# Kernel optimization log

Measured on AMD Instinct MI355X. Metric: run time of the kernel, lower is better.

The kernel has to match this reference:

```python
import jax, jax.numpy as jnp
import numpy as np

# hyperparameters from init_kwargs
TEMP = 0.05
MOMENTUM = 0.2
ALPHA = 0.9
TEMP_DIST = 0.6
LAMBDA1 = 1.0
LAMBDA2 = 1.0
EPS_CONS = 2.0
NUM_SAMPLES = 8192
NUM_FEATURES = 2048
B = 256
K = 20
EPS = 1e-12


def setup_inputs() -> dict:
    key = jax.random.key(0)
    ks = jax.random.split(key, 8)
    inputs0 = jax.random.normal(ks[0], (B, NUM_FEATURES), dtype=jnp.float32)
    logits0 = jax.random.normal(ks[1], (B, NUM_SAMPLES), dtype=jnp.float32)
    logits1 = jax.random.normal(ks[2], (B, NUM_SAMPLES), dtype=jnp.float32)
    targets = jax.random.randint(ks[3], (B,), 0, NUM_SAMPLES, dtype=jnp.int32)
    indexes = jnp.arange(B, dtype=jnp.int32)  # global idx == batch idx (identity idx2bidx)
    neighbors = jax.random.randint(ks[4], (B, K), 0, B, dtype=jnp.int32)
    neighbor_dists = jax.random.uniform(ks[5], (B, K), dtype=jnp.float32)
    rampup = jnp.ones((), dtype=jnp.float32)
    features = jax.random.normal(ks[6], (NUM_SAMPLES, NUM_FEATURES), dtype=jnp.float32)
    features = features / jnp.linalg.norm(features, axis=1, keepdims=True)
    return {
        'inputs0': inputs0, 'logits0': logits0, 'logits1': logits1,
        'targets': targets, 'indexes': indexes, 'neighbors': neighbors,
        'neighbor_dists': neighbor_dists, 'rampup': rampup, 'features': features,
    }


def reference(inputs0, logits0, logits1, targets, indexes, neighbors,
              neighbor_dists, rampup, features):
    # F.normalize(inputs[0], dim=1)
    x = inputs0 / jnp.maximum(jnp.linalg.norm(inputs0, axis=1, keepdims=True), EPS)

    # CM forward: scores against memory bank, scaled by temperature
    outputs = (x @ features.T) / TEMP                      # [B, S]
    logp = jax.nn.log_softmax(outputs, axis=-1)
    loss_nce = -jnp.mean(jnp.take_along_axis(logp, targets[:, None], axis=1))

    targets_onehot = jax.nn.one_hot(targets, NUM_SAMPLES, dtype=logits0.dtype)

    # neighbor gathering: indexes = arange(B) so idx2bidx is identity; every
    # neighbor in [0,B) passes the `nb in indexes` filter.
    p0 = jax.nn.softmax(logits0, axis=-1)[neighbors]       # [B, K, S]
    p1 = jax.nn.softmax(logits1, axis=-1)[neighbors]       # [B, K, S]
    # loop appends logits0-row then logits1-row per neighbor -> interleave
    p = jnp.stack([p0, p1], axis=2).reshape(B, 2 * K, NUM_SAMPLES)
    d2 = jnp.repeat(neighbor_dists, 2, axis=1)             # [B, 2K] (d,d pairs)
    w = jax.nn.softmax(d2 / TEMP_DIST, axis=1)             # [B, 2K]
    logits_neighbors1 = jnp.einsum('bk,bks->bs', w, p)     # [B, S]

    # KL branch: neighbors with dist <= eps_consistency (all, since eps=2.0)
    mask = (neighbor_dists <= EPS_CONS).astype(p0.dtype)   # [B, K]
    cnt = jnp.maximum(mask.sum(axis=1, keepdims=True), 1.0)
    logits_neighbors1_KL = jnp.einsum('bk,bks->bs', mask, p0) / cnt  # [B, S]

    refined = ALPHA * targets_onehot + (1.0 - ALPHA) * jax.lax.stop_gradient(logits_neighbors1)
    loss_ce = jnp.mean(jnp.sum(-refined * jax.nn.log_softmax(logits0, axis=-1), axis=1))

    # KLDivLoss(logsoftmax(logits1).detach(), target) with batchmean reduction
    lp1 = jax.lax.stop_gradient(jax.nn.log_softmax(logits1, axis=-1))
    t = logits_neighbors1_KL
    kl = jnp.sum(jnp.where(t > 0, t * (jnp.log(jnp.maximum(t, EPS)) - lp1), 0.0)) / B

    # CM momentum memory-bank scatter update (backward side-effect in torch);
    # equivalent to the sequential loop when targets are unique in the batch.
    upd = MOMENTUM * features[targets] + (1.0 - MOMENTUM) * x
    upd = upd / jnp.maximum(jnp.linalg.norm(upd, axis=1, keepdims=True), EPS)
    new_features = features.at[targets].set(upd)

    return (loss_nce, LAMBDA1 * loss_ce, LAMBDA2 * rampup * kl, new_features)
```

## Files before the change

### kernel.cpp

```cpp
#include <hip/hip_runtime.h>
#include <cmath>

#define NB 256
#define NS 8192
#define NF 2048
#define NK 20

typedef _Float16 half8 __attribute__((ext_vector_type(8)));
typedef _Float16 half4 __attribute__((ext_vector_type(4)));
typedef float f32x4 __attribute__((ext_vector_type(4)));

__device__ __forceinline__ void async16(const void* g, void* l) {
  __builtin_amdgcn_global_load_lds(
      (const __attribute__((address_space(1))) unsigned int*)g,
      (__attribute__((address_space(3))) unsigned int*)l, 16, 0, 0);
}

__device__ __forceinline__ float waveSum(float v) {
#pragma unroll
  for (int off = 32; off > 0; off >>= 1) v += __shfl_xor(v, off, 64);
  return v;
}
__device__ __forceinline__ float waveMax(float v) {
#pragma unroll
  for (int off = 32; off > 0; off >>= 1) v = fmaxf(v, __shfl_xor(v, off, 64));
  return v;
}

__global__ __launch_bounds__(256) void prep(
    const float* __restrict__ in0, const float* __restrict__ logits0,
    const float* __restrict__ logits1, _Float16* __restrict__ P,
    _Float16* __restrict__ xh, float* __restrict__ alpha,
    float* __restrict__ mll, float* __restrict__ loss) {
  __shared__ float redA[4], redB[4];
  int tid = threadIdx.x, blk = blockIdx.x;
  int wave = tid >> 6, lane = tid & 63;

  if (blk < 512) {
    if (blk == 0 && tid < 3) loss[tid] = 0.0f;
    int r = blk;
    const float* src = (r < NB) ? logits0 : logits1;
    const float4* row = (const float4*)(src + (size_t)(r & (NB - 1)) * NS);
    float4 v[8];
    float mx = -1e30f;
#pragma unroll
    for (int i = 0; i < 8; ++i) {
      v[i] = row[tid + i * 256];
      mx = fmaxf(mx, fmaxf(fmaxf(v[i].x, v[i].y), fmaxf(v[i].z, v[i].w)));
    }
    float wv = waveMax(mx);
    if (lane == 0) redA[wave] = wv;
    __syncthreads();
    float m = fmaxf(fmaxf(redA[0], redA[1]), fmaxf(redA[2], redA[3]));
    float em = expf(m);
    float se = 0.0f;
    half4* prow = (half4*)(P + (size_t)r * NS);
#pragma unroll
    for (int i = 0; i < 8; ++i) {
      float e0 = expf(v[i].x - m), e1 = expf(v[i].y - m);
      float e2 = expf(v[i].z - m), e3 = expf(v[i].w - m);
      se += (e0 + e1) + (e2 + e3);
      half4 h;
      h[0] = (_Float16)(e0 * em); h[1] = (_Float16)(e1 * em);
      h[2] = (_Float16)(e2 * em); h[3] = (_Float16)(e3 * em);
      prow[tid + i * 256] = h;
    }
    float sw = waveSum(se);
    if (lane == 0) redB[wave] = sw;
    __syncthreads();
    float l = (redB[0] + redB[1]) + (redB[2] + redB[3]);
    if (tid == 0) {
      mll[r] = m + logf(l);
      alpha[r] = 256.0f * expf(-m) / l;
    }
  } else {
    int b = blk - 512;
    const float4* row = (const float4*)(in0 + (size_t)b * NF);
    float4 v0 = row[tid], v1 = row[tid + 256];
    float ss = v0.x * v0.x + v0.y * v0.y + v0.z * v0.z + v0.w * v0.w +
               v1.x * v1.x + v1.y * v1.y + v1.z * v1.z + v1.w * v1.w;
    float w = waveSum(ss);
    if (lane == 0) redA[wave] = w;
    __syncthreads();
    float tot = (redA[0] + redA[1]) + (redA[2] + redA[3]);
    float inv = 1.0f / fmaxf(sqrtf(tot), 1e-12f);
    half4 h0, h1;
    h0[0] = (_Float16)(v0.x * inv); h0[1] = (_Float16)(v0.y * inv);
    h0[2] = (_Float16)(v0.z * inv); h0[3] = (_Float16)(v0.w * inv);
    h1[0] = (_Float16)(v1.x * inv); h1[1] = (_Float16)(v1.y * inv);
    h1[2] = (_Float16)(v1.z * inv); h1[3] = (_Float16)(v1.w * inv);
    ((half4*)(xh + (size_t)b * NF))[tid] = h0;
    ((half4*)(xh + (size_t)b * NF))[tid + 256] = h1;
  }
}

__global__ __launch_bounds__(256) void fused2(
    const _Float16* __restrict__ xh, const float* __restrict__ fB,
    const _Float16* __restrict__ P, const float* __restrict__ alpha,
    const float* __restrict__ mll, const float* __restrict__ logits0,
    const float* __restrict__ logits1, const int* __restrict__ targets,
    const int* __restrict__ neighbors, const float* __restrict__ ndist,
    const float* __restrict__ rampup, float* __restrict__ outF,
    float* __restrict__ pm, float* __restrict__ pl, float* __restrict__ tgt,
    float* __restrict__ out) {
  __shared__ alignas(16) _Float16 As[128 * 64];
  __shared__ alignas(16) _Float16 Bs[64 * 64];
  __shared__ float red[8];
  int tid = threadIdx.x, wave = tid >> 6, lane = tid & 63;
  int quad = lane >> 4, r16 = lane & 15;
  int blk = blockIdx.x;

  if (blk < 256) {
    int bx = blk & 127, by = blk >> 7;
    int n0 = bx * 64, m0 = by * 128;
    int brow = tid >> 2, bcg = tid & 3;
    f32x4 acc[2][4] = {};
    for (int k0 = 0; k0 < NF; k0 += 64) {
      float4 fv[4];
      const float* bsrc = fB + (size_t)(n0 + brow) * NF + k0 + bcg * 16;
#pragma unroll
      for (int q = 0; q < 4; ++q) fv[q] = *(const float4*)(bsrc + q * 4);
      __syncthreads();
#pragma unroll
      for (int ss = 0; ss < 4; ++ss) {
        int rl = ss * 32 + (tid >> 3);
        int sc = (tid & 7) ^ (rl & 7);
        async16(xh + (size_t)(m0 + rl) * NF + k0 + sc * 8,
                &As[rl * 64 + (tid & 7) * 8]);
      }
#pragma unroll
      for (int h = 0; h < 2; ++h) {
        half8 hh;
        hh[0] = (_Float16)fv[2 * h].x; hh[1] = (_Float16)fv[2 * h].y;
        hh[2] = (_Float16)fv[2 * h].z; hh[3] = (_Float16)fv[2 * h].w;
        hh[4] = (_Float16)fv[2 * h + 1].x; hh[5] = (_Float16)fv[2 * h + 1].y;
        hh[6] = (_Float16)fv[2 * h + 1].z; hh[7] = (_Float16)fv[2 * h + 1].w;
        int c8 = bcg * 2 + h;
        *(half8*)&Bs[brow * 64 + ((c8 ^ (brow & 7)) << 3)] = hh;
      }
      __syncthreads();
      if (by == (k0 >= NF / 2)) {
        float4* odst = (float4*)(outF + (size_t)(n0 + brow) * NF + k0 + bcg * 16);
#pragma unroll
        for (int q = 0; q < 4; ++q) odst[q] = fv[q];
      }
#pragma unroll
      for (int sub = 0; sub < 2; ++sub) {
        int slot = ((sub * 4 + quad) ^ (r16 & 7)) * 8;
        half8 af[2], bf[4];
#pragma unroll
        for (int i = 0; i < 2; ++i)
          af[i] = *(const half8*)&As[(wave * 32 + i * 16 + r16) * 64 + slot];
#pragma unroll
        for (int j = 0; j < 4; ++j)
          bf[j] = *(const half8*)&Bs[(j * 16 + r16) * 64 + slot];
#pragma unroll
        for (int i = 0; i < 2; ++i)
#pragma unroll
          for (int j = 0; j < 4; ++j)
            acc[i][j] = __builtin_amdgcn_mfma_f32_16x16x32_f16(af[i], bf[j], acc[i][j], 0, 0, 0);
      }
    }
#pragma unroll
    for (int i = 0; i < 2; ++i)
#pragma unroll
      for (int r = 0; r < 4; ++r) {
        int R = m0 + wave * 32 + i * 16 + quad * 4 + r;
        float sv[4];
#pragma unroll
        for (int j = 0; j < 4; ++j) sv[j] = acc[i][j][r] * 20.0f;
        float mx = fmaxf(fmaxf(sv[0], sv[1]), fmaxf(sv[2], sv[3]));
#pragma unroll
        for (int m2 = 1; m2 < 16; m2 <<= 1) mx = fmaxf(mx, __shfl_xor(mx, m2, 64));
        float e = expf(sv[0] - mx) + expf(sv[1] - mx) + expf(sv[2] - mx) + expf(sv[3] - mx);
#pragma unroll
        for (int m2 = 1; m2 < 16; m2 <<= 1) e += __shfl_xor(e, m2, 64);
        int tg = targets[R];
#pragma unroll
        for (int j = 0; j < 4; ++j)
          if (n0 + j * 16 + r16 == tg) tgt[R] = sv[j];
        if (r16 == 0) { pm[R * 128 + bx] = mx; pl[R * 128 + bx] = e; }
      }
  } else {
    int gb = blk - 256;
    int b = gb >> 2, s0 = (gb & 3) * 2048;
    float s = 0.0f;
    int cnt = 0;
#pragma unroll
    for (int k = 0; k < NK; ++k) {
      float d = ndist[b * NK + k];
      s += expf(d * (1.0f / 0.6f));
      cnt += (d <= 2.0f) ? 1 : 0;
    }
    float invs = 1.0f / (2.0f * s);
    float invc = 1.0f / fmaxf((float)cnt, 1.0f);
    float ce[8] = {0, 0, 0, 0, 0, 0, 0, 0};
    float kl[8] = {0, 0, 0, 0, 0, 0, 0, 0};
    int sc_ = s0 + tid * 8;
#pragma unroll 4
    for (int k = 0; k < NK; ++k) {
      float d = ndist[b * NK + k];
      int n = neighbors[b * NK + k];
      float wce = expf(d * (1.0f / 0.6f)) * invs;
      float wkl = (d <= 2.0f) ? invc : 0.0f;
      float a0 = alpha[n], a1 = alpha[256 + n];
      float c0 = wce * a0, c1 = wce * a1, ck = wkl * a0;
      half8 p0 = *(const half8*)(P + (size_t)n * NS + sc_);
      half8 p1 = *(const half8*)(P + (size_t)(256 + n) * NS + sc_);
#pragma unroll
      for (int e2 = 0; e2 < 8; ++e2) {
        float q0 = (float)p0[e2], q1 = (float)p1[e2];
        ce[e2] += c0 * q0 + c1 * q1;
        kl[e2] += ck * q0;
      }
    }
    float mv0 = mll[b], mv1 = mll[256 + b];
    const float* g0 = logits0 + (size_t)b * NS + sc_;
    const float* g1 = logits1 + (size_t)b * NS + sc_;
    float4 l0a = *(const float4*)g0, l0b = *(const float4*)(g0 + 4);
    float4 l1a = *(const float4*)g1, l1b = *(const float4*)(g1 + 4);
    float lg0[8] = {l0a.x, l0a.y, l0a.z, l0a.w, l0b.x, l0b.y, l0b.z, l0b.w};
    float lg1[8] = {l1a.x, l1a.y, l1a.z, l1a.w, l1b.x, l1b.y, l1b.z, l1b.w};
    float lce = 0.0f, lkl = 0.0f;
#pragma unroll
    for (int e2 = 0; e2 < 8; ++e2) {
      float t = ce[e2] * (1.0f / 256.0f);
      lce += t * (lg0[e2] - mv0);
      float tk = kl[e2] * (1.0f / 256.0f);
      lkl += (tk > 0.0f) ? tk * (logf(fmaxf(tk, 1e-12f)) - (lg1[e2] - mv1)) : 0.0f;
    }
    float wc = waveSum(lce), wk = waveSum(lkl);
    if (lane == 0) { red[wave] = wc; red[4 + wave] = wk; }
    __syncthreads();
    if (tid == 0) {
      float ce_t = (red[0] + red[1]) + (red[2] + red[3]);
      float kl_t = (red[4] + red[5]) + (red[6] + red[7]);
      atomicAdd(out + 1, -0.1f * ce_t * (1.0f / 256.0f));
      atomicAdd(out + 2, rampup[0] * kl_t * (1.0f / 256.0f));
    }
  }
}

__global__ __launch_bounds__(128) void final_reduce(
    const float* __restrict__ pm, const float* __restrict__ pl,
    const float* __restrict__ tgt, const float* __restrict__ logits0,
    const float* __restrict__ mll, const int* __restrict__ targets,
    const float* __restrict__ in0, const float* __restrict__ features,
    float* __restrict__ outF, float* __restrict__ out) {
  __shared__ float rA[2], rB[2];
  __shared__ int flag;
  int tid = threadIdx.x, blk = blockIdx.x;
  if (blk < 256) {
    int b = blk;
    float m = pm[b * 128 + tid];
    float l = pl[b * 128 + tid];
    float wm = waveMax(m);
    if ((tid & 63) == 0) rA[tid >> 6] = wm;
    __syncthreads();
    float mx = fmaxf(rA[0], rA[1]);
    float e = l * expf(m - mx);
    float ws = waveSum(e);
    if ((tid & 63) == 0) rB[tid >> 6] = ws;
    __syncthreads();
    if (tid == 0) {
      float S = rB[0] + rB[1];
      float nce = -(tgt[b] - mx - logf(S));
      int tg = targets[b];
      float oh = -0.9f * (logits0[(size_t)b * NS + tg] - mll[b]);
      atomicAdd(out + 0, nce * (1.0f / 256.0f));
      atomicAdd(out + 1, oh * (1.0f / 256.0f));
    }
  } else {
    int b = blk - 256;
    int tg = targets[b];
    if (tid == 0) flag = 0;
    __syncthreads();
    bool later = false;
    for (int i = b + 1 + tid; i < 256; i += 128) later = later || (targets[i] == tg);
    if (later) flag = 1;
    __syncthreads();
    if (flag) return;
    const float4* xr = (const float4*)(in0 + (size_t)b * NF);
    const float4* fr = (const float4*)(features + (size_t)tg * NF);
    float4 a[4];
    float ssx = 0.0f;
#pragma unroll
    for (int s = 0; s < 4; ++s) {
      a[s] = xr[tid + s * 128];
      ssx += a[s].x * a[s].x + a[s].y * a[s].y + a[s].z * a[s].z + a[s].w * a[s].w;
    }
    float w1 = waveSum(ssx);
    if ((tid & 63) == 0) rA[tid >> 6] = w1;
    __syncthreads();
    float ix = 0.8f / fmaxf(sqrtf(rA[0] + rA[1]), 1e-12f);
    float4 v[4];
    float ss = 0.0f;
#pragma unroll
    for (int s = 0; s < 4; ++s) {
      float4 f = fr[tid + s * 128];
      v[s] = make_float4(0.2f * f.x + ix * a[s].x, 0.2f * f.y + ix * a[s].y,
                         0.2f * f.z + ix * a[s].z, 0.2f * f.w + ix * a[s].w);
      ss += v[s].x * v[s].x + v[s].y * v[s].y + v[s].z * v[s].z + v[s].w * v[s].w;
    }
    float w2 = waveSum(ss);
    if ((tid & 63) == 0) rB[tid >> 6] = w2;
    __syncthreads();
    float inv = 1.0f / fmaxf(sqrtf(rB[0] + rB[1]), 1e-12f);
    float4* o4 = (float4*)(outF + (size_t)tg * NF);
#pragma unroll
    for (int s = 0; s < 4; ++s)
      o4[tid + s * 128] = make_float4(v[s].x * inv, v[s].y * inv, v[s].z * inv, v[s].w * inv);
  }
}

extern "C" void kernel_launch(void* const* d_in, const int* in_sizes, int n_in,
                              void* d_out, int out_size, void* d_ws, size_t ws_size,
                              hipStream_t stream) {
  const float* inputs0 = (const float*)d_in[0];
  const float* logits0 = (const float*)d_in[1];
  const float* logits1 = (const float*)d_in[2];
  const int* targets = (const int*)d_in[3];
  const int* neighbors = (const int*)d_in[5];
  const float* ndist = (const float*)d_in[6];
  const float* rampup = (const float*)d_in[7];
  const float* features = (const float*)d_in[8];
  float* out = (float*)d_out;

  char* ws = (char*)d_ws;
  float* mll = (float*)(ws + 4096);
  float* alpha = (float*)(ws + 8192);
  float* tgt = (float*)(ws + 16384);
  float* pm = (float*)(ws + 65536);
  float* pl = (float*)(ws + 196608);
  _Float16* xh = (_Float16*)(ws + (3 << 20));
  _Float16* P = (_Float16*)(ws + (4 << 20));

  prep<<<768, 256, 0, stream>>>(inputs0, logits0, logits1, P, xh, alpha, mll, out);
  fused2<<<1280, 256, 0, stream>>>(xh, features, P, alpha, mll, logits0, logits1,
                                   targets, neighbors, ndist, rampup, out + 3,
                                   pm, pl, tgt, out);
  final_reduce<<<512, 128, 0, stream>>>(pm, pl, tgt, logits0, mll, targets,
                                        inputs0, features, out + 3, out);
}
```

Measured before the change: 204.7 us.

## Double-buffer GEMM tiles in LDS and remap blocks for L2 locality

The GEMM main loop now uses two LDS buffers for the A and B tiles. The next k-slice's global loads and async LDS copies are issued before the current slice's MFMAs, and there is one barrier per iteration instead of two. Block indices are also remapped so that the two row-halves (by=0/1) sharing the same feature columns run adjacently, to improve L2 reuse of the fp32 feature bank. LDS use doubles, which may reduce occupancy.

```diff
diff --git a/kernel.cpp b/kernel.cpp
--- a/kernel.cpp
+++ b/kernel.cpp
@@ -103,31 +103,31 @@
     const float* __restrict__ rampup, float* __restrict__ outF,
     float* __restrict__ pm, float* __restrict__ pl, float* __restrict__ tgt,
     float* __restrict__ out) {
-  __shared__ alignas(16) _Float16 As[128 * 64];
-  __shared__ alignas(16) _Float16 Bs[64 * 64];
+  __shared__ alignas(16) _Float16 As[2][128 * 64];
+  __shared__ alignas(16) _Float16 Bs[2][64 * 64];
   __shared__ float red[8];
   int tid = threadIdx.x, wave = tid >> 6, lane = tid & 63;
   int quad = lane >> 4, r16 = lane & 15;
   int blk = blockIdx.x;
 
   if (blk < 256) {
-    int bx = blk & 127, by = blk >> 7;
+    int by = (blk >> 3) & 1;
+    int bx = (blk & 7) | ((blk >> 4) << 3);
     int n0 = bx * 64, m0 = by * 128;
     int brow = tid >> 2, bcg = tid & 3;
-    f32x4 acc[2][4] = {};
-    for (int k0 = 0; k0 < NF; k0 += 64) {
-      float4 fv[4];
-      const float* bsrc = fB + (size_t)(n0 + brow) * NF + k0 + bcg * 16;
-#pragma unroll
-      for (int q = 0; q < 4; ++q) fv[q] = *(const float4*)(bsrc + q * 4);
-      __syncthreads();
+    const float* bsrc = fB + (size_t)(n0 + brow) * NF + bcg * 16;
+
+    auto loadA = [&](int kel, int bufi) {
 #pragma unroll
       for (int ss = 0; ss < 4; ++ss) {
         int rl = ss * 32 + (tid >> 3);
         int sc = (tid & 7) ^ (rl & 7);
-        async16(xh + (size_t)(m0 + rl) * NF + k0 + sc * 8,
-                &As[rl * 64 + (tid & 7) * 8]);
-      }
+        async16(xh + (size_t)(m0 + rl) * NF + kel + sc * 8,
+                &As[bufi][rl * 64 + (tid & 7) * 8]);
+      }
+    };
+    float4 fv[4];
+    auto writeB = [&](int bufi) {
 #pragma unroll
       for (int h = 0; h < 2; ++h) {
         half8 hh;
@@ -136,13 +136,30 @@
         hh[4] = (_Float16)fv[2 * h + 1].x; hh[5] = (_Float16)fv[2 * h + 1].y;
         hh[6] = (_Float16)fv[2 * h + 1].z; hh[7] = (_Float16)fv[2 * h + 1].w;
         int c8 = bcg * 2 + h;
-        *(half8*)&Bs[brow * 64 + ((c8 ^ (brow & 7)) << 3)] = hh;
-      }
-      __syncthreads();
-      if (by == (k0 >= NF / 2)) {
-        float4* odst = (float4*)(outF + (size_t)(n0 + brow) * NF + k0 + bcg * 16);
-#pragma unroll
-        for (int q = 0; q < 4; ++q) odst[q] = fv[q];
+        *(half8*)&Bs[bufi][brow * 64 + ((c8 ^ (brow & 7)) << 3)] = hh;
+      }
+    };
+    auto storeO = [&](int kel) {
+      float4* odst = (float4*)(outF + (size_t)(n0 + brow) * NF + kel + bcg * 16);
+#pragma unroll
+      for (int q = 0; q < 4; ++q) odst[q] = fv[q];
+    };
+
+    f32x4 acc[2][4] = {};
+#pragma unroll
+    for (int q = 0; q < 4; ++q) fv[q] = *(const float4*)(bsrc + q * 4);
+    loadA(0, 0);
+    writeB(0);
+    if (by == 0) storeO(0);
+    __syncthreads();
+
+    for (int k = 0; k < 32; ++k) {
+      int buf = k & 1;
+      int kn = (k + 1) * 64;
+      if (kn < NF) {
+#pragma unroll
+        for (int q = 0; q < 4; ++q) fv[q] = *(const float4*)(bsrc + kn + q * 4);
+        loadA(kn, buf ^ 1);
       }
 #pragma unroll
       for (int sub = 0; sub < 2; ++sub) {
@@ -150,15 +167,20 @@
         half8 af[2], bf[4];
 #pragma unroll
         for (int i = 0; i < 2; ++i)
-          af[i] = *(const half8*)&As[(wave * 32 + i * 16 + r16) * 64 + slot];
+          af[i] = *(const half8*)&As[buf][(wave * 32 + i * 16 + r16) * 64 + slot];
 #pragma unroll
         for (int j = 0; j < 4; ++j)
-          bf[j] = *(const half8*)&Bs[(j * 16 + r16) * 64 + slot];
+          bf[j] = *(const half8*)&Bs[buf][(j * 16 + r16) * 64 + slot];
 #pragma unroll
         for (int i = 0; i < 2; ++i)
 #pragma unroll
           for (int j = 0; j < 4; ++j)
             acc[i][j] = __builtin_amdgcn_mfma_f32_16x16x32_f16(af[i], bf[j], acc[i][j], 0, 0, 0);
+      }
+      if (kn < NF) {
+        writeB(buf ^ 1);
+        if (by == (kn >= NF / 2 ? 1 : 0)) storeO(kn);
+        __syncthreads();
       }
     }
 #pragma unroll
```

Result: no change. 207.1 us (+1.2%).

## Halve GEMM N-tile to double blocks and prefetch next feature slice

Applied to the files above, without the earlier changes.

The GEMM part of the fused kernel now uses 32-column feature tiles instead of 64, launching 512 GEMM blocks instead of 256 to spread the memory-bound feature read across more CUs. It also loads the next k-slice of features into registers during the current iteration's MFMA work, and remaps block indices so blocks sharing a feature tile run near each other. Partial softmax stats double to 256 per row, so the workspace layout and the final reduce are updated to match. The cost is halved MFMA work per A-tile load, so the xh operand is re-read twice as often.

```diff
diff --git a/kernel.cpp b/kernel.cpp
--- a/kernel.cpp
+++ b/kernel.cpp
@@ -104,22 +104,25 @@
     float* __restrict__ pm, float* __restrict__ pl, float* __restrict__ tgt,
     float* __restrict__ out) {
   __shared__ alignas(16) _Float16 As[128 * 64];
-  __shared__ alignas(16) _Float16 Bs[64 * 64];
+  __shared__ alignas(16) _Float16 Bs[32 * 64];
   __shared__ float red[8];
   int tid = threadIdx.x, wave = tid >> 6, lane = tid & 63;
   int quad = lane >> 4, r16 = lane & 15;
   int blk = blockIdx.x;
 
-  if (blk < 256) {
-    int bx = blk & 127, by = blk >> 7;
-    int n0 = bx * 64, m0 = by * 128;
-    int brow = tid >> 2, bcg = tid & 3;
-    f32x4 acc[2][4] = {};
+  if (blk < 512) {
+    int by = (blk >> 3) & 1;
+    int bx = (blk & 7) | ((blk >> 4) << 3);
+    int n0 = bx * 32, m0 = by * 128;
+    int brow = tid >> 3, bq = tid & 7;
+    const float* bsrc = fB + (size_t)(n0 + brow) * NF + bq * 8;
+
+    float4 fv[2];
+    f32x4 acc[2][2] = {};
+    fv[0] = *(const float4*)bsrc;
+    fv[1] = *(const float4*)(bsrc + 4);
+
     for (int k0 = 0; k0 < NF; k0 += 64) {
-      float4 fv[4];
-      const float* bsrc = fB + (size_t)(n0 + brow) * NF + k0 + bcg * 16;
-#pragma unroll
-      for (int q = 0; q < 4; ++q) fv[q] = *(const float4*)(bsrc + q * 4);
       __syncthreads();
 #pragma unroll
       for (int ss = 0; ss < 4; ++ss) {
@@ -128,36 +131,38 @@
         async16(xh + (size_t)(m0 + rl) * NF + k0 + sc * 8,
                 &As[rl * 64 + (tid & 7) * 8]);
       }
-#pragma unroll
-      for (int h = 0; h < 2; ++h) {
+      {
         half8 hh;
-        hh[0] = (_Float16)fv[2 * h].x; hh[1] = (_Float16)fv[2 * h].y;
-        hh[2] = (_Float16)fv[2 * h].z; hh[3] = (_Float16)fv[2 * h].w;
-        hh[4] = (_Float16)fv[2 * h + 1].x; hh[5] = (_Float16)fv[2 * h + 1].y;
-        hh[6] = (_Float16)fv[2 * h + 1].z; hh[7] = (_Float16)fv[2 * h + 1].w;
-        int c8 = bcg * 2 + h;
-        *(half8*)&Bs[brow * 64 + ((c8 ^ (brow & 7)) << 3)] = hh;
+        hh[0] = (_Float16)fv[0].x; hh[1] = (_Float16)fv[0].y;
+        hh[2] = (_Float16)fv[0].z; hh[3] = (_Float16)fv[0].w;
+        hh[4] = (_Float16)fv[1].x; hh[5] = (_Float16)fv[1].y;
+        hh[6] = (_Float16)fv[1].z; hh[7] = (_Float16)fv[1].w;
+        *(half8*)&Bs[brow * 64 + ((bq ^ (brow & 7)) << 3)] = hh;
       }
       __syncthreads();
-      if (by == (k0 >= NF / 2)) {
-        float4* odst = (float4*)(outF + (size_t)(n0 + brow) * NF + k0 + bcg * 16);
-#pragma unroll
-        for (int q = 0; q < 4; ++q) odst[q] = fv[q];
+      if (by == (k0 >= NF / 2 ? 1 : 0)) {
+        float4* o = (float4*)(outF + (size_t)(n0 + brow) * NF + k0 + bq * 8);
+        o[0] = fv[0];
+        o[1] = fv[1];
+      }
+      if (k0 + 64 < NF) {
+        fv[0] = *(const float4*)(bsrc + k0 + 64);
+        fv[1] = *(const float4*)(bsrc + k0 + 68);
       }
 #pragma unroll
       for (int sub = 0; sub < 2; ++sub) {
         int slot = ((sub * 4 + quad) ^ (r16 & 7)) * 8;
-        half8 af[2], bf[4];
+        half8 af[2], bf[2];
 #pragma unroll
         for (int i = 0; i < 2; ++i)
           af[i] = *(const half8*)&As[(wave * 32 + i * 16 + r16) * 64 + slot];
 #pragma unroll
-        for (int j = 0; j < 4; ++j)
+        for (int j = 0; j < 2; ++j)
           bf[j] = *(const half8*)&Bs[(j * 16 + r16) * 64 + slot];
 #pragma unroll
         for (int i = 0; i < 2; ++i)
 #pragma unroll
-          for (int j = 0; j < 4; ++j)
+          for (int j = 0; j < 2; ++j)
             acc[i][j] = __builtin_amdgcn_mfma_f32_16x16x32_f16(af[i], bf[j], acc[i][j], 0, 0, 0);
       }
     }
@@ -166,23 +171,20 @@
 #pragma unroll
       for (int r = 0; r < 4; ++r) {
         int R = m0 + wave * 32 + i * 16 + quad * 4 + r;
-        float sv[4];
-#pragma unroll
-        for (int j = 0; j < 4; ++j) sv[j] = acc[i][j][r] * 20.0f;
-        float mx = fmaxf(fmaxf(sv[0], sv[1]), fmaxf(sv[2], sv[3]));
+        float s0 = acc[i][0][r] * 20.0f, s1 = acc[i][1][r] * 20.0f;
+        float mx = fmaxf(s0, s1);
 #pragma unroll
         for (int m2 = 1; m2 < 16; m2 <<= 1) mx = fmaxf(mx, __shfl_xor(mx, m2, 64));
-        float e = expf(sv[0] - mx) + expf(sv[1] - mx) + expf(sv[2] - mx) + expf(sv[3] - mx);
+        float e = expf(s0 - mx) + expf(s1 - mx);
 #pragma unroll
         for (int m2 = 1; m2 < 16; m2 <<= 1) e += __shfl_xor(e, m2, 64);
         int tg = targets[R];
-#pragma unroll
-        for (int j = 0; j < 4; ++j)
-          if (n0 + j * 16 + r16 == tg) tgt[R] = sv[j];
-        if (r16 == 0) { pm[R * 128 + bx] = mx; pl[R * 128 + bx] = e; }
+        if (n0 + r16 == tg) tgt[R] = s0;
+        if (n0 + 16 + r16 == tg) tgt[R] = s1;
+        if (r16 == 0) { pm[R * 256 + bx] = mx; pl[R * 256 + bx] = e; }
       }
   } else {
-    int gb = blk - 256;
+    int gb = blk - 512;
     int b = gb >> 2, s0 = (gb & 3) * 2048;
     float s = 0.0f;
     int cnt = 0;
@@ -252,13 +254,13 @@
   int tid = threadIdx.x, blk = blockIdx.x;
   if (blk < 256) {
     int b = blk;
-    float m = pm[b * 128 + tid];
-    float l = pl[b * 128 + tid];
-    float wm = waveMax(m);
+    float m1 = pm[b * 256 + tid], m2v = pm[b * 256 + 128 + tid];
+    float l1 = pl[b * 256 + tid], l2v = pl[b * 256 + 128 + tid];
+    float wm = waveMax(fmaxf(m1, m2v));
     if ((tid & 63) == 0) rA[tid >> 6] = wm;
     __syncthreads();
     float mx = fmaxf(rA[0], rA[1]);
-    float e = l * expf(m - mx);
+    float e = l1 * expf(m1 - mx) + l2v * expf(m2v - mx);
     float ws = waveSum(e);
     if ((tid & 63) == 0) rB[tid >> 6] = ws;
     __syncthreads();
@@ -331,12 +333,12 @@
   float* alpha = (float*)(ws + 8192);
   float* tgt = (float*)(ws + 16384);
   float* pm = (float*)(ws + 65536);
-  float* pl = (float*)(ws + 196608);
+  float* pl = (float*)(ws + 65536 + 262144);
   _Float16* xh = (_Float16*)(ws + (3 << 20));
   _Float16* P = (_Float16*)(ws + (4 << 20));
 
   prep<<<768, 256, 0, stream>>>(inputs0, logits0, logits1, P, xh, alpha, mll, out);
-  fused2<<<1280, 256, 0, stream>>>(xh, features, P, alpha, mll, logits0, logits1,
+  fused2<<<1536, 256, 0, stream>>>(xh, features, P, alpha, mll, logits0, logits1,
                                    targets, neighbors, ndist, rampup, out + 3,
                                    pm, pl, tgt, out);
   final_reduce<<<512, 128, 0, stream>>>(pm, pl, tgt, logits0, mll, targets,
```

Measured after the change: 199.5 us. -2.6%, faster.
